# Optimization experiments

Hardware: AMD Instinct MI355X
Metric: run time of the kernel (lower is better)

## Reference

```python
import jax, jax.numpy as jnp
import numpy as np

B, C, H, W = 16, 64, 128, 128
K = 3  # dynamic kernel size


def setup_inputs() -> dict:
    key = jax.random.key(0)
    ks = jax.random.split(key, 6)
    return {
        "x": jax.random.normal(ks[0], (B, C, H, W), jnp.float32),       # feature map
        "d": jax.random.normal(ks[1], (B, 64), jnp.float32),            # degradation repr
        "Wk1": jax.random.normal(ks[2], (64, 64), jnp.float32) * 0.05,  # Linear(64,64), no bias
        "Wk2": jax.random.normal(ks[3], (64 * K * K, 64), jnp.float32) * 0.05,  # Linear(64,576)
        "Wc": jax.random.normal(ks[4], (64, 64), jnp.float32) * 0.05,   # 1x1 conv weight (out,in)
        "bc": jnp.zeros((64,), jnp.float32),                            # 1x1 conv bias
    }


def _lrelu(v):
    return jnp.where(v >= 0, v, 0.1 * v)


def reference(x, d, Wk1, Wk2, Wc, bc):
    b, c, h, w = x.shape
    k = K
    # kernel-generating MLP: Linear -> LeakyReLU(0.1) -> Linear
    hid = _lrelu(d @ Wk1.T)                      # (B, 64)
    kern = (hid @ Wk2.T).reshape(b, c, 1, k, k)   # one 3x3 kernel per (batch, channel)

    # dynamic depthwise 3x3 conv: per-sample kernels, groups == channels
    def dwconv(xi, ki):
        # xi: (C,H,W), ki: (C,1,3,3) in OIHW with feature_group_count=C
        return jax.lax.conv_general_dilated(
            xi[None], ki, window_strides=(1, 1), padding='SAME',
            feature_group_count=c,
            dimension_numbers=('NCHW', 'OIHW', 'NCHW'))[0]

    out = jax.vmap(dwconv)(x, kern)              # (B,C,H,W)
    out = _lrelu(out)
    # 1x1 pointwise conv with bias
    out = jnp.einsum('bchw,oc->bohw', out, Wc) + bc[None, :, None, None]
    return out
```

## Files before the change

### kernel.cpp

```cpp
#include <hip/hip_runtime.h>

#define Bn 16
#define Cn 64
#define Hn 128
#define Wn 128
#define HWn (Hn * Wn)

typedef __attribute__((ext_vector_type(8)))  short  short8;
typedef __attribute__((ext_vector_type(16))) float  floatx16;
typedef __attribute__((ext_vector_type(4)))  float  floatx4;
using int32x4 = int __attribute__((ext_vector_type(4)));

__device__ floatx4
llvm_amdgcn_raw_buffer_load_v4f32(int32x4 srsrc, int voffset, int soffset,
                                  int aux) __asm("llvm.amdgcn.raw.buffer.load.v4f32");

__device__ __forceinline__ int32x4 make_rsrc(const void* p, int bytes) {
    int32x4 r;
    r.x = (int)(unsigned)(uintptr_t)p;
    r.y = (int)((uintptr_t)p >> 32);
    r.z = bytes;
    r.w = 0x00020000;
    return r;
}

__device__ __forceinline__ unsigned short f2bf(float f) {
    unsigned u = __float_as_uint(f);
    u += 0x7fffu + ((u >> 16) & 1u);
    return (unsigned short)(u >> 16);
}
__device__ __forceinline__ float lrelu(float v) { return v >= 0.f ? v : 0.1f * v; }

#define SYNC_LDS() asm volatile("s_waitcnt lgkmcnt(0)\n\ts_barrier" ::: "memory")

__global__ __launch_bounds__(192)
void gen_kern7(const float* __restrict__ d,
               const float* __restrict__ Wk1,
               const float* __restrict__ Wk2,
               const float* __restrict__ Wc,
               float* __restrict__ kernP,
               unsigned short* __restrict__ WcT) {
    const int b = blockIdx.x;
    const int r = blockIdx.y;
    const int t = threadIdx.x;
    __shared__ float hid_s[64];

    if (t < 64) {
        const float4* __restrict__ w4 = (const float4*)(Wk1 + (size_t)t * 64);
        const float*  __restrict__ db = d + b * 64;
        float s0 = 0.f, s1 = 0.f, s2 = 0.f, s3 = 0.f;
        #pragma unroll
        for (int j = 0; j < 16; ++j) {
            const float4 wv = w4[j];
            s0 += db[4 * j + 0] * wv.x;
            s1 += db[4 * j + 1] * wv.y;
            s2 += db[4 * j + 2] * wv.z;
            s3 += db[4 * j + 3] * wv.w;
        }
        hid_s[t] = lrelu((s0 + s1) + (s2 + s3));
    }
    __syncthreads();

    {
        const int o = r * 192 + t;
        const float4* __restrict__ w4 = (const float4*)(Wk2 + (size_t)o * 64);
        const float4* __restrict__ h4 = (const float4*)hid_s;
        float s0 = 0.f, s1 = 0.f, s2 = 0.f, s3 = 0.f;
        #pragma unroll
        for (int j = 0; j < 16; ++j) {
            const float4 wv = w4[j];
            const float4 hv = h4[j];
            s0 += hv.x * wv.x;
            s1 += hv.y * wv.y;
            s2 += hv.z * wv.z;
            s3 += hv.w * wv.w;
        }
        const int c = o / 9, tap = o - c * 9;
        kernP[b * 768 + c * 12 + tap] = (s0 + s1) + (s2 + s3);
    }

    if (b == 0 && r == 0) {
        for (int idx = t; idx < 4096; idx += 192) {
            const int j    = idx & 7;
            const int lane = (idx >> 3) & 63;
            const int g    = (idx >> 9) & 3;
            const int m    = idx >> 11;
            const int col  = lane & 31, kh = lane >> 5;
            const int o    = m * 32 + col;
            const int c    = g * 16 + kh * 8 + j;
            WcT[idx] = f2bf(Wc[o * 64 + c]);
        }
    }
}

struct XK { floatx4 x[3][2]; };
struct KF { floatx4 k0, k1; float k8; };

__device__ __forceinline__ void issue_x(XK& v, int32x4 rs, int c,
                                        const int* rofsB, int px0) {
    #pragma unroll
    for (int r = 0; r < 3; ++r) {
        const int vo = (c << 16) + rofsB[r] + px0 * 4;
        v.x[r][0] = llvm_amdgcn_raw_buffer_load_v4f32(rs, vo, 0, 0);
        v.x[r][1] = llvm_amdgcn_raw_buffer_load_v4f32(rs, vo + 16, 0, 0);
    }
}

__device__ __forceinline__ void issue_k(KF& kf, const float* kp, int c) {
    const floatx4* k4 = (const floatx4*)(kp + c * 12);
    kf.k0 = k4[0];
    kf.k1 = k4[1];
    kf.k8 = ((const float*)k4)[8];
}

__device__ __forceinline__ short8 compute_dw(const XK& v, const KF& kf,
                                             int lane, int tm) {
    float t0[8], t1[8], t2[8];
    #pragma unroll
    for (int i = 0; i < 8; ++i) {
        const float xr0 = (i < 4) ? v.x[0][0][i] : v.x[0][1][i - 4];
        const float xr1 = (i < 4) ? v.x[1][0][i] : v.x[1][1][i - 4];
        const float xr2 = (i < 4) ? v.x[2][0][i] : v.x[2][1][i - 4];
        t0[i] = kf.k0.x * xr0 + kf.k0.w * xr1 + kf.k1.z * xr2;
        t1[i] = kf.k0.y * xr0 + kf.k1.x * xr1 + kf.k1.w * xr2;
        t2[i] = kf.k0.z * xr0 + kf.k1.y * xr1 + kf.k8   * xr2;
    }
    float t0m = __shfl(t0[7], lane - 1, 64);
    float t2p = __shfl(t2[0], lane + 1, 64);
    if (tm == 0)  t0m = 0.f;
    if (tm == 15) t2p = 0.f;

    float dw[8];
    dw[0] = t0m + t1[0] + t2[1];
    #pragma unroll
    for (int i = 1; i < 7; ++i) dw[i] = t0[i - 1] + t1[i] + t2[i + 1];
    dw[7] = t0[6] + t1[7] + t2p;

    short8 w8;
    #pragma unroll
    for (int i = 0; i < 8; ++i) w8[i] = (short)f2bf(lrelu(dw[i]));
    return w8;
}

__global__ __launch_bounds__(256, 4)
void da_mfma5(const float* __restrict__ x,
              const float* __restrict__ kernP,
              const unsigned short* __restrict__ WcT,
              const float* __restrict__ bc,
              float* __restrict__ out) {
    const int t    = threadIdx.x;
    const int lane = t & 63;
    const int wv   = t >> 6;
    const int col  = lane & 31;
    const int kh   = lane >> 5;
    const int bx   = blockIdx.x;
    const int h    = ((bx & 7) << 4) | (bx >> 3);
    const int b    = blockIdx.y;
    const int px   = wv * 32 + col;

    const int sch = t >> 4;
    const int tm  = t & 15;
    const int px0 = tm * 8;

    __shared__ unsigned short dwB[2][2048];

    int rofsB[3];
    #pragma unroll
    for (int i = 0; i < 3; ++i) {
        const int hh = h + i - 1;
        rofsB[i] = (hh >= 0 && hh < Hn) ? hh * (Wn * 4) : 0x10000000;
    }

    const int32x4 rs = make_rsrc(x + (size_t)b * Cn * HWn, Cn * HWn * 4);
    const float* __restrict__ kp = kernP + b * 768;

    floatx16 acc[2];
    #pragma unroll
    for (int m = 0; m < 2; ++m)
        #pragma unroll
        for (int r = 0; r < 16; ++r)
            acc[m][r] = 0.f;

    XK X[4]; KF Kf[4]; short8 a0[4], a1[4];
    a0[0] = *(const short8*)(WcT + ((0 * 4 + 0) * 64 + lane) * 8);
    a1[0] = *(const short8*)(WcT + ((1 * 4 + 0) * 64 + lane) * 8);
    issue_k(Kf[0], kp, sch);
    issue_k(Kf[1], kp, 16 + sch);
    issue_x(X[0], rs, sch, rofsB, px0);
    issue_x(X[1], rs, 16 + sch, rofsB, px0);
    {
        const short8 w8 = compute_dw(X[0], Kf[0], lane, tm);
        *(short8*)&dwB[0][sch * 128 + (px0 ^ ((sch & 8) << 2))] = w8;
    }
    SYNC_LDS();

    #pragma unroll
    for (int g = 0; g < 4; ++g) {
        if (g < 2) issue_x(X[g + 2], rs, (g + 2) * 16 + sch, rofsB, px0);
        if (g < 3) {
            a0[g + 1] = *(const short8*)(WcT + ((0 * 4 + g + 1) * 64 + lane) * 8);
            a1[g + 1] = *(const short8*)(WcT + ((1 * 4 + g + 1) * 64 + lane) * 8);
        }
        if (g < 2) issue_k(Kf[g + 2], kp, (g + 2) * 16 + sch);

        short8 bfr;
        #pragma unroll
        for (int j = 0; j < 8; ++j) {
            const int cl = kh * 8 + j;
            bfr[j] = (short)dwB[g & 1][cl * 128 + (px ^ ((cl & 8) << 2))];
        }
        acc[0] = __builtin_amdgcn_mfma_f32_32x32x16_bf16(a0[g], bfr, acc[0], 0, 0, 0);
        acc[1] = __builtin_amdgcn_mfma_f32_32x32x16_bf16(a1[g], bfr, acc[1], 0, 0, 0);

        if (g < 3) {
            const short8 w8 = compute_dw(X[g + 1], Kf[g + 1], lane, tm);
            *(short8*)&dwB[(g + 1) & 1][sch * 128 + (px0 ^ ((sch & 8) << 2))] = w8;
            SYNC_LDS();
        }
    }

    float* __restrict__ ob = out + (size_t)b * Cn * HWn + h * Wn + px;
    #pragma unroll
    for (int m = 0; m < 2; ++m)
        #pragma unroll
        for (int q = 0; q < 4; ++q) {
            const float4 bv = *(const float4*)&bc[m * 32 + q * 8 + 4 * kh];
            #pragma unroll
            for (int j = 0; j < 4; ++j) {
                const int o = m * 32 + q * 8 + 4 * kh + j;
                ob[(size_t)o * HWn] = acc[m][q * 4 + j] + ((const float*)&bv)[j];
            }
        }
}

extern "C" void kernel_launch(void* const* d_in, const int* in_sizes, int n_in,
                              void* d_out, int out_size, void* d_ws, size_t ws_size,
                              hipStream_t stream) {
    const float* x   = (const float*)d_in[0];
    const float* d   = (const float*)d_in[1];
    const float* Wk1 = (const float*)d_in[2];
    const float* Wk2 = (const float*)d_in[3];
    const float* Wc  = (const float*)d_in[4];
    const float* bc  = (const float*)d_in[5];
    float* out = (float*)d_out;
    float*          kernP = (float*)d_ws;
    unsigned short* WcT   = (unsigned short*)((float*)d_ws + Bn * 768);

    gen_kern7<<<dim3(Bn, 3), dim3(192), 0, stream>>>(d, Wk1, Wk2, Wc, kernP, WcT);
    da_mfma5<<<dim3(Hn, Bn), dim3(256), 0, stream>>>(x, kernP, WcT, bc, out);
}
```

Measured before the change: 137.7 us.

## Make depthwise stage wave-local to drop block barriers and cross-lane shuffles

Each wave now computes the depthwise conv for exactly the 32 pixels it later feeds into its own MFMA, using a per-wave LDS slice, so the block-wide barriers between stages go away. The horizontal halo is obtained with two extra scalar buffer loads per row instead of lane shuffles. Prefetch depth drops from four channel groups to a double buffer, and the weight fragments and dynamic kernels are loaded per iteration rather than ahead of time. The aim is to remove barrier stalls and shuffle overhead, at the cost of redundant halo loads and less memory latency hiding. It also relies on intra-wave LDS ordering without an explicit wait.

Result: slower. 164.5 us (+19.5%).

```diff
diff --git a/kernel.cpp b/kernel.cpp
--- a/kernel.cpp
+++ b/kernel.cpp
@@ -11,6 +11,9 @@
 typedef __attribute__((ext_vector_type(4)))  float  floatx4;
 using int32x4 = int __attribute__((ext_vector_type(4)));
 
+__device__ float
+llvm_amdgcn_raw_buffer_load_fp32(int32x4 srsrc, int voffset, int soffset,
+                                 int aux) __asm("llvm.amdgcn.raw.buffer.load.f32");
 __device__ floatx4
 llvm_amdgcn_raw_buffer_load_v4f32(int32x4 srsrc, int voffset, int soffset,
                                   int aux) __asm("llvm.amdgcn.raw.buffer.load.v4f32");
@@ -30,8 +33,6 @@
     return (unsigned short)(u >> 16);
 }
 __device__ __forceinline__ float lrelu(float v) { return v >= 0.f ? v : 0.1f * v; }
-
-#define SYNC_LDS() asm volatile("s_waitcnt lgkmcnt(0)\n\ts_barrier" ::: "memory")
 
 __global__ __launch_bounds__(192)
 void gen_kern7(const float* __restrict__ d,
@@ -93,16 +94,19 @@
     }
 }
 
-struct XK { floatx4 x[3][2]; };
+struct XK { floatx4 v[3][2]; float xl[3], xh[3]; };
 struct KF { floatx4 k0, k1; float k8; };
 
-__device__ __forceinline__ void issue_x(XK& v, int32x4 rs, int c,
-                                        const int* rofsB, int px0) {
+__device__ __forceinline__ void issue_x(XK& X, int32x4 rs, int c,
+                                        const int* rofsB, int px0b,
+                                        int loOfs, int hiOfs) {
     #pragma unroll
     for (int r = 0; r < 3; ++r) {
-        const int vo = (c << 16) + rofsB[r] + px0 * 4;
-        v.x[r][0] = llvm_amdgcn_raw_buffer_load_v4f32(rs, vo, 0, 0);
-        v.x[r][1] = llvm_amdgcn_raw_buffer_load_v4f32(rs, vo + 16, 0, 0);
+        const int base = (c << 16) + rofsB[r];
+        X.v[r][0] = llvm_amdgcn_raw_buffer_load_v4f32(rs, base + px0b, 0, 0);
+        X.v[r][1] = llvm_amdgcn_raw_buffer_load_v4f32(rs, base + px0b + 16, 0, 0);
+        X.xl[r]   = llvm_amdgcn_raw_buffer_load_fp32 (rs, base + loOfs, 0, 0);
+        X.xh[r]   = llvm_amdgcn_raw_buffer_load_fp32 (rs, base + hiOfs, 0, 0);
     }
 }
 
@@ -113,22 +117,19 @@
     kf.k8 = ((const float*)k4)[8];
 }
 
-__device__ __forceinline__ short8 compute_dw(const XK& v, const KF& kf,
-                                             int lane, int tm) {
+__device__ __forceinline__ short8 compute_dw(const XK& X, const KF& kf) {
     float t0[8], t1[8], t2[8];
     #pragma unroll
     for (int i = 0; i < 8; ++i) {
-        const float xr0 = (i < 4) ? v.x[0][0][i] : v.x[0][1][i - 4];
-        const float xr1 = (i < 4) ? v.x[1][0][i] : v.x[1][1][i - 4];
-        const float xr2 = (i < 4) ? v.x[2][0][i] : v.x[2][1][i - 4];
+        const float xr0 = (i < 4) ? X.v[0][0][i] : X.v[0][1][i - 4];
+        const float xr1 = (i < 4) ? X.v[1][0][i] : X.v[1][1][i - 4];
+        const float xr2 = (i < 4) ? X.v[2][0][i] : X.v[2][1][i - 4];
         t0[i] = kf.k0.x * xr0 + kf.k0.w * xr1 + kf.k1.z * xr2;
         t1[i] = kf.k0.y * xr0 + kf.k1.x * xr1 + kf.k1.w * xr2;
         t2[i] = kf.k0.z * xr0 + kf.k1.y * xr1 + kf.k8   * xr2;
     }
-    float t0m = __shfl(t0[7], lane - 1, 64);
-    float t2p = __shfl(t2[0], lane + 1, 64);
-    if (tm == 0)  t0m = 0.f;
-    if (tm == 15) t2p = 0.f;
+    const float t0m = kf.k0.x * X.xl[0] + kf.k0.w * X.xl[1] + kf.k1.z * X.xl[2];
+    const float t2p = kf.k0.z * X.xh[0] + kf.k1.y * X.xh[1] + kf.k8   * X.xh[2];
 
     float dw[8];
     dw[0] = t0m + t1[0] + t2[1];
@@ -143,7 +144,7 @@
 }
 
 __global__ __launch_bounds__(256, 4)
-void da_mfma5(const float* __restrict__ x,
+void da_mfma6(const float* __restrict__ x,
               const float* __restrict__ kernP,
               const unsigned short* __restrict__ WcT,
               const float* __restrict__ bc,
@@ -158,11 +159,11 @@
     const int b    = blockIdx.y;
     const int px   = wv * 32 + col;
 
-    const int sch = t >> 4;
-    const int tm  = t & 15;
-    const int px0 = tm * 8;
-
-    __shared__ unsigned short dwB[2][2048];
+    const int sc   = lane & 15;
+    const int oct  = lane >> 4;
+    const int px0  = wv * 32 + oct * 8;
+
+    __shared__ unsigned short dwS[4][2][16][32];
 
     int rofsB[3];
     #pragma unroll
@@ -170,6 +171,9 @@
         const int hh = h + i - 1;
         rofsB[i] = (hh >= 0 && hh < Hn) ? hh * (Wn * 4) : 0x10000000;
     }
+    const int loOfs = (px0 - 1 >= 0) ? (px0 - 1) * 4 : 0x10000000;
+    const int hiOfs = (px0 + 8 < Wn) ? (px0 + 8) * 4 : 0x10000000;
+    const int px0b  = px0 * 4;
 
     const int32x4 rs = make_rsrc(x + (size_t)b * Cn * HWn, Cn * HWn * 4);
     const float* __restrict__ kp = kernP + b * 768;
@@ -181,42 +185,30 @@
         for (int r = 0; r < 16; ++r)
             acc[m][r] = 0.f;
 
-    XK X[4]; KF Kf[4]; short8 a0[4], a1[4];
-    a0[0] = *(const short8*)(WcT + ((0 * 4 + 0) * 64 + lane) * 8);
-    a1[0] = *(const short8*)(WcT + ((1 * 4 + 0) * 64 + lane) * 8);
-    issue_k(Kf[0], kp, sch);
-    issue_k(Kf[1], kp, 16 + sch);
-    issue_x(X[0], rs, sch, rofsB, px0);
-    issue_x(X[1], rs, 16 + sch, rofsB, px0);
-    {
-        const short8 w8 = compute_dw(X[0], Kf[0], lane, tm);
-        *(short8*)&dwB[0][sch * 128 + (px0 ^ ((sch & 8) << 2))] = w8;
-    }
-    SYNC_LDS();
+    XK X[2];
+    issue_x(X[0], rs, sc, rofsB, px0b, loOfs, hiOfs);
 
     #pragma unroll
     for (int g = 0; g < 4; ++g) {
-        if (g < 2) issue_x(X[g + 2], rs, (g + 2) * 16 + sch, rofsB, px0);
-        if (g < 3) {
-            a0[g + 1] = *(const short8*)(WcT + ((0 * 4 + g + 1) * 64 + lane) * 8);
-            a1[g + 1] = *(const short8*)(WcT + ((1 * 4 + g + 1) * 64 + lane) * 8);
-        }
-        if (g < 2) issue_k(Kf[g + 2], kp, (g + 2) * 16 + sch);
+        const int cur = g & 1, nxt = cur ^ 1;
+        if (g < 3)
+            issue_x(X[nxt], rs, (g + 1) * 16 + sc, rofsB, px0b, loOfs, hiOfs);
+
+        const short8 a0 = *(const short8*)(WcT + ((0 * 4 + g) * 64 + lane) * 8);
+        const short8 a1 = *(const short8*)(WcT + ((1 * 4 + g) * 64 + lane) * 8);
+
+        KF kf;
+        issue_k(kf, kp, g * 16 + sc);
+        const short8 w8 = compute_dw(X[cur], kf);
+        *(short8*)&dwS[wv][cur][sc][oct * 8] = w8;
 
         short8 bfr;
         #pragma unroll
-        for (int j = 0; j < 8; ++j) {
-            const int cl = kh * 8 + j;
-            bfr[j] = (short)dwB[g & 1][cl * 128 + (px ^ ((cl & 8) << 2))];
-        }
-        acc[0] = __builtin_amdgcn_mfma_f32_32x32x16_bf16(a0[g], bfr, acc[0], 0, 0, 0);
-        acc[1] = __builtin_amdgcn_mfma_f32_32x32x16_bf16(a1[g], bfr, acc[1], 0, 0, 0);
-
-        if (g < 3) {
-            const short8 w8 = compute_dw(X[g + 1], Kf[g + 1], lane, tm);
-            *(short8*)&dwB[(g + 1) & 1][sch * 128 + (px0 ^ ((sch & 8) << 2))] = w8;
-            SYNC_LDS();
-        }
+        for (int j = 0; j < 8; ++j)
+            bfr[j] = (short)dwS[wv][cur][kh * 8 + j][col];
+
+        acc[0] = __builtin_amdgcn_mfma_f32_32x32x16_bf16(a0, bfr, acc[0], 0, 0, 0);
+        acc[1] = __builtin_amdgcn_mfma_f32_32x32x16_bf16(a1, bfr, acc[1], 0, 0, 0);
     }
 
     float* __restrict__ ob = out + (size_t)b * Cn * HWn + h * Wn + px;
@@ -247,5 +239,5 @@
     unsigned short* WcT   = (unsigned short*)((float*)d_ws + Bn * 768);
 
     gen_kern7<<<dim3(Bn, 3), dim3(192), 0, stream>>>(d, Wk1, Wk2, Wc, kernP, WcT);
-    da_mfma5<<<dim3(Hn, Bn), dim3(256), 0, stream>>>(x, kernP, WcT, bc, out);
-}
+    da_mfma6<<<dim3(Hn, Bn), dim3(256), 0, stream>>>(x, kernP, WcT, bc, out);
+}
```

## Restructure depthwise-MFMA pipeline into two phases of two channel groups

Applied to the files above, without the earlier changes.

Replaces the four-stage one-group-ahead software pipeline with two phases, each computing the depthwise result for two channel groups into separate LDS slices before a single barrier and two MFMA steps. The loads for the second pair of groups are issued after the first phase's compute, behind a scheduling barrier. This halves the number of LDS barriers and reduces register arrays for prefetched inputs, at the cost of less overlap between global loads and compute and doubled LDS usage.

After: 136.2 us. No clear change (-1.1%).

```diff
diff --git a/kernel.cpp b/kernel.cpp
--- a/kernel.cpp
+++ b/kernel.cpp
@@ -143,7 +143,7 @@
 }
 
 __global__ __launch_bounds__(256, 4)
-void da_mfma5(const float* __restrict__ x,
+void da_mfma7(const float* __restrict__ x,
               const float* __restrict__ kernP,
               const unsigned short* __restrict__ WcT,
               const float* __restrict__ bc,
@@ -162,7 +162,7 @@
     const int tm  = t & 15;
     const int px0 = tm * 8;
 
-    __shared__ unsigned short dwB[2][2048];
+    __shared__ unsigned short dwS[2][2][2048];
 
     int rofsB[3];
     #pragma unroll
@@ -181,41 +181,49 @@
         for (int r = 0; r < 16; ++r)
             acc[m][r] = 0.f;
 
-    XK X[4]; KF Kf[4]; short8 a0[4], a1[4];
-    a0[0] = *(const short8*)(WcT + ((0 * 4 + 0) * 64 + lane) * 8);
-    a1[0] = *(const short8*)(WcT + ((1 * 4 + 0) * 64 + lane) * 8);
+    XK X[2]; KF Kf[2];
     issue_k(Kf[0], kp, sch);
     issue_k(Kf[1], kp, 16 + sch);
     issue_x(X[0], rs, sch, rofsB, px0);
     issue_x(X[1], rs, 16 + sch, rofsB, px0);
-    {
-        const short8 w8 = compute_dw(X[0], Kf[0], lane, tm);
-        *(short8*)&dwB[0][sch * 128 + (px0 ^ ((sch & 8) << 2))] = w8;
-    }
-    SYNC_LDS();
-
-    #pragma unroll
-    for (int g = 0; g < 4; ++g) {
-        if (g < 2) issue_x(X[g + 2], rs, (g + 2) * 16 + sch, rofsB, px0);
-        if (g < 3) {
-            a0[g + 1] = *(const short8*)(WcT + ((0 * 4 + g + 1) * 64 + lane) * 8);
-            a1[g + 1] = *(const short8*)(WcT + ((1 * 4 + g + 1) * 64 + lane) * 8);
-        }
-        if (g < 2) issue_k(Kf[g + 2], kp, (g + 2) * 16 + sch);
-
-        short8 bfr;
-        #pragma unroll
-        for (int j = 0; j < 8; ++j) {
-            const int cl = kh * 8 + j;
-            bfr[j] = (short)dwB[g & 1][cl * 128 + (px ^ ((cl & 8) << 2))];
-        }
-        acc[0] = __builtin_amdgcn_mfma_f32_32x32x16_bf16(a0[g], bfr, acc[0], 0, 0, 0);
-        acc[1] = __builtin_amdgcn_mfma_f32_32x32x16_bf16(a1[g], bfr, acc[1], 0, 0, 0);
-
-        if (g < 3) {
-            const short8 w8 = compute_dw(X[g + 1], Kf[g + 1], lane, tm);
-            *(short8*)&dwB[(g + 1) & 1][sch * 128 + (px0 ^ ((sch & 8) << 2))] = w8;
-            SYNC_LDS();
+
+    #pragma unroll
+    for (int ph = 0; ph < 2; ++ph) {
+        short8 a0s[2], a1s[2];
+        #pragma unroll
+        for (int s = 0; s < 2; ++s) {
+            const int g = ph * 2 + s;
+            a0s[s] = *(const short8*)(WcT + ((0 * 4 + g) * 64 + lane) * 8);
+            a1s[s] = *(const short8*)(WcT + ((1 * 4 + g) * 64 + lane) * 8);
+        }
+
+        {
+            const short8 w0 = compute_dw(X[0], Kf[0], lane, tm);
+            *(short8*)&dwS[ph][0][sch * 128 + (px0 ^ ((sch & 8) << 2))] = w0;
+            const short8 w1 = compute_dw(X[1], Kf[1], lane, tm);
+            *(short8*)&dwS[ph][1][sch * 128 + (px0 ^ ((sch & 8) << 2))] = w1;
+        }
+
+        if (ph == 0) {
+            issue_x(X[0], rs, 2 * 16 + sch, rofsB, px0);
+            issue_x(X[1], rs, 3 * 16 + sch, rofsB, px0);
+            issue_k(Kf[0], kp, 2 * 16 + sch);
+            issue_k(Kf[1], kp, 3 * 16 + sch);
+            __builtin_amdgcn_sched_barrier(0);
+        }
+
+        SYNC_LDS();
+
+        #pragma unroll
+        for (int s = 0; s < 2; ++s) {
+            short8 bfr;
+            #pragma unroll
+            for (int j = 0; j < 8; ++j) {
+                const int cl = kh * 8 + j;
+                bfr[j] = (short)dwS[ph][s][cl * 128 + (px ^ ((cl & 8) << 2))];
+            }
+            acc[0] = __builtin_amdgcn_mfma_f32_32x32x16_bf16(a0s[s], bfr, acc[0], 0, 0, 0);
+            acc[1] = __builtin_amdgcn_mfma_f32_32x32x16_bf16(a1s[s], bfr, acc[1], 0, 0, 0);
         }
     }
 
@@ -247,5 +255,5 @@
     unsigned short* WcT   = (unsigned short*)((float*)d_ws + Bn * 768);
 
     gen_kern7<<<dim3(Bn, 3), dim3(192), 0, stream>>>(d, Wk1, Wk2, Wc, kernP, WcT);
-    da_mfma5<<<dim3(Hn, Bn), dim3(256), 0, stream>>>(x, kernP, WcT, bc, out);
-}
+    da_mfma7<<<dim3(Hn, Bn), dim3(256), 0, stream>>>(x, kernP, WcT, bc, out);
+}
```

## Stage x rows into LDS via async global_load_lds with double buffering

Applied to the files above, without the earlier changes.

Replaces the register-resident buffer loads of the three input rows with direct global-to-LDS asynchronous loads into a double-buffered shared tile, pipelined across channel groups with vmcnt waits. Out-of-range rows are clamped to a valid row and then zeroed in LDS. All Wc fragments and per-channel kernels are loaded up front, and the launch-bounds occupancy hint drops from 4 to 2. The aim is to cut VGPR pressure and overlap loads with compute, at the cost of much more LDS per block (about 65 KB), which may limit occupancy. There is a possible race: one group's zero-fill writes are not separated by a barrier from other waves reading that buffer.

Result: no change. 138.1 us (+0.3%).

```diff
diff --git a/kernel.cpp b/kernel.cpp
--- a/kernel.cpp
+++ b/kernel.cpp
@@ -9,20 +9,6 @@
 typedef __attribute__((ext_vector_type(8)))  short  short8;
 typedef __attribute__((ext_vector_type(16))) float  floatx16;
 typedef __attribute__((ext_vector_type(4)))  float  floatx4;
-using int32x4 = int __attribute__((ext_vector_type(4)));
-
-__device__ floatx4
-llvm_amdgcn_raw_buffer_load_v4f32(int32x4 srsrc, int voffset, int soffset,
-                                  int aux) __asm("llvm.amdgcn.raw.buffer.load.v4f32");
-
-__device__ __forceinline__ int32x4 make_rsrc(const void* p, int bytes) {
-    int32x4 r;
-    r.x = (int)(unsigned)(uintptr_t)p;
-    r.y = (int)((uintptr_t)p >> 32);
-    r.z = bytes;
-    r.w = 0x00020000;
-    return r;
-}
 
 __device__ __forceinline__ unsigned short f2bf(float f) {
     unsigned u = __float_as_uint(f);
@@ -32,6 +18,10 @@
 __device__ __forceinline__ float lrelu(float v) { return v >= 0.f ? v : 0.1f * v; }
 
 #define SYNC_LDS() asm volatile("s_waitcnt lgkmcnt(0)\n\ts_barrier" ::: "memory")
+#define WAIT_VM(N) asm volatile("s_waitcnt vmcnt(" #N ")" ::: "memory")
+
+typedef const __attribute__((address_space(1))) void* as1cv;
+typedef __attribute__((address_space(3))) void*       as3v;
 
 __global__ __launch_bounds__(192)
 void gen_kern7(const float* __restrict__ d,
@@ -96,23 +86,6 @@
 struct XK { floatx4 x[3][2]; };
 struct KF { floatx4 k0, k1; float k8; };
 
-__device__ __forceinline__ void issue_x(XK& v, int32x4 rs, int c,
-                                        const int* rofsB, int px0) {
-    #pragma unroll
-    for (int r = 0; r < 3; ++r) {
-        const int vo = (c << 16) + rofsB[r] + px0 * 4;
-        v.x[r][0] = llvm_amdgcn_raw_buffer_load_v4f32(rs, vo, 0, 0);
-        v.x[r][1] = llvm_amdgcn_raw_buffer_load_v4f32(rs, vo + 16, 0, 0);
-    }
-}
-
-__device__ __forceinline__ void issue_k(KF& kf, const float* kp, int c) {
-    const floatx4* k4 = (const floatx4*)(kp + c * 12);
-    kf.k0 = k4[0];
-    kf.k1 = k4[1];
-    kf.k8 = ((const float*)k4)[8];
-}
-
 __device__ __forceinline__ short8 compute_dw(const XK& v, const KF& kf,
                                              int lane, int tm) {
     float t0[8], t1[8], t2[8];
@@ -142,8 +115,8 @@
     return w8;
 }
 
-__global__ __launch_bounds__(256, 4)
-void da_mfma5(const float* __restrict__ x,
+__global__ __launch_bounds__(256, 2)
+void da_mfma8(const float* __restrict__ x,
               const float* __restrict__ kernP,
               const unsigned short* __restrict__ WcT,
               const float* __restrict__ bc,
@@ -159,20 +132,36 @@
     const int px   = wv * 32 + col;
 
     const int sch = t >> 4;
-    const int tm  = t & 15;
-    const int px0 = tm * 8;
-
-    __shared__ unsigned short dwB[2][2048];
-
-    int rofsB[3];
+    const int oct = t & 15;
+    const int px0 = oct * 8;
+
+    __shared__ float xS[2][24][256];
+    __shared__ unsigned short dwS[4][2048];
+
+    int hh[3];
     #pragma unroll
     for (int i = 0; i < 3; ++i) {
-        const int hh = h + i - 1;
-        rofsB[i] = (hh >= 0 && hh < Hn) ? hh * (Wn * 4) : 0x10000000;
-    }
-
-    const int32x4 rs = make_rsrc(x + (size_t)b * Cn * HWn, Cn * HWn * 4);
+        const int hr = h + i - 1;
+        hh[i] = (hr < 0) ? h : (hr >= Hn ? h : hr);
+    }
+    const bool oobTop = (h == 0);
+    const bool oobBot = (h == Hn - 1);
+
+    const float* __restrict__ xb = x + (size_t)b * Cn * HWn;
     const float* __restrict__ kp = kernP + b * 768;
+
+    auto dma_group = [&](int g) {
+        float (&buf)[24][256] = xS[g & 1];
+        #pragma unroll
+        for (int r = 0; r < 3; ++r) {
+            const float* gs = xb + (size_t)(g * 16 + sch) * HWn
+                                 + (size_t)hh[r] * Wn + px0;
+            __builtin_amdgcn_global_load_lds((as1cv)gs,
+                (as3v)&buf[(r * 2 + 0) * 4 + wv][0], 16, 0, 0);
+            __builtin_amdgcn_global_load_lds((as1cv)(gs + 4),
+                (as3v)&buf[(r * 2 + 1) * 4 + wv][0], 16, 0, 0);
+        }
+    };
 
     floatx16 acc[2];
     #pragma unroll
@@ -181,42 +170,55 @@
         for (int r = 0; r < 16; ++r)
             acc[m][r] = 0.f;
 
-    XK X[4]; KF Kf[4]; short8 a0[4], a1[4];
-    a0[0] = *(const short8*)(WcT + ((0 * 4 + 0) * 64 + lane) * 8);
-    a1[0] = *(const short8*)(WcT + ((1 * 4 + 0) * 64 + lane) * 8);
-    issue_k(Kf[0], kp, sch);
-    issue_k(Kf[1], kp, 16 + sch);
-    issue_x(X[0], rs, sch, rofsB, px0);
-    issue_x(X[1], rs, 16 + sch, rofsB, px0);
-    {
-        const short8 w8 = compute_dw(X[0], Kf[0], lane, tm);
-        *(short8*)&dwB[0][sch * 128 + (px0 ^ ((sch & 8) << 2))] = w8;
-    }
-    SYNC_LDS();
-
+    dma_group(0);
+    short8 a0s[4], a1s[4]; KF Kf[4];
     #pragma unroll
     for (int g = 0; g < 4; ++g) {
-        if (g < 2) issue_x(X[g + 2], rs, (g + 2) * 16 + sch, rofsB, px0);
-        if (g < 3) {
-            a0[g + 1] = *(const short8*)(WcT + ((0 * 4 + g + 1) * 64 + lane) * 8);
-            a1[g + 1] = *(const short8*)(WcT + ((1 * 4 + g + 1) * 64 + lane) * 8);
-        }
-        if (g < 2) issue_k(Kf[g + 2], kp, (g + 2) * 16 + sch);
+        a0s[g] = *(const short8*)(WcT + ((0 * 4 + g) * 64 + lane) * 8);
+        a1s[g] = *(const short8*)(WcT + ((1 * 4 + g) * 64 + lane) * 8);
+        const floatx4* k4 = (const floatx4*)(kp + (g * 16 + sch) * 12);
+        Kf[g].k0 = k4[0];
+        Kf[g].k1 = k4[1];
+        Kf[g].k8 = ((const float*)k4)[8];
+    }
+    dma_group(1);
+
+    #pragma unroll
+    for (int g = 0; g < 4; ++g) {
+        if (g >= 1 && g <= 2) dma_group(g + 1);
+        if (g < 3) WAIT_VM(6); else WAIT_VM(0);
+
+        const int tb = g & 1;
+        if (oobTop) {
+            const floatx4 z = {0.f, 0.f, 0.f, 0.f};
+            *((floatx4*)&xS[tb][0 + wv][0] + lane) = z;
+            *((floatx4*)&xS[tb][4 + wv][0] + lane) = z;
+        }
+        if (oobBot) {
+            const floatx4 z = {0.f, 0.f, 0.f, 0.f};
+            *((floatx4*)&xS[tb][16 + wv][0] + lane) = z;
+            *((floatx4*)&xS[tb][20 + wv][0] + lane) = z;
+        }
+
+        XK v;
+        #pragma unroll
+        for (int r = 0; r < 3; ++r) {
+            v.x[r][0] = *((const floatx4*)&xS[tb][(r * 2 + 0) * 4 + wv][0] + lane);
+            v.x[r][1] = *((const floatx4*)&xS[tb][(r * 2 + 1) * 4 + wv][0] + lane);
+        }
+        const short8 w8 = compute_dw(v, Kf[g], lane, oct);
+        *(short8*)&dwS[g][sch * 128 + (px0 ^ ((sch & 8) << 2))] = w8;
+
+        SYNC_LDS();
 
         short8 bfr;
         #pragma unroll
         for (int j = 0; j < 8; ++j) {
             const int cl = kh * 8 + j;
-            bfr[j] = (short)dwB[g & 1][cl * 128 + (px ^ ((cl & 8) << 2))];
-        }
-        acc[0] = __builtin_amdgcn_mfma_f32_32x32x16_bf16(a0[g], bfr, acc[0], 0, 0, 0);
-        acc[1] = __builtin_amdgcn_mfma_f32_32x32x16_bf16(a1[g], bfr, acc[1], 0, 0, 0);
-
-        if (g < 3) {
-            const short8 w8 = compute_dw(X[g + 1], Kf[g + 1], lane, tm);
-            *(short8*)&dwB[(g + 1) & 1][sch * 128 + (px0 ^ ((sch & 8) << 2))] = w8;
-            SYNC_LDS();
-        }
+            bfr[j] = (short)dwS[g][cl * 128 + (px ^ ((cl & 8) << 2))];
+        }
+        acc[0] = __builtin_amdgcn_mfma_f32_32x32x16_bf16(a0s[g], bfr, acc[0], 0, 0, 0);
+        acc[1] = __builtin_amdgcn_mfma_f32_32x32x16_bf16(a1s[g], bfr, acc[1], 0, 0, 0);
     }
 
     float* __restrict__ ob = out + (size_t)b * Cn * HWn + h * Wn + px;
@@ -247,5 +249,5 @@
     unsigned short* WcT   = (unsigned short*)((float*)d_ws + Bn * 768);
 
     gen_kern7<<<dim3(Bn, 3), dim3(192), 0, stream>>>(d, Wk1, Wk2, Wc, kernP, WcT);
-    da_mfma5<<<dim3(Hn, Bn), dim3(256), 0, stream>>>(x, kernP, WcT, bc, out);
-}
+    da_mfma8<<<dim3(Hn, Bn), dim3(256), 0, stream>>>(x, kernP, WcT, bc, out);
+}
```
